# Kernel optimization log

Hardware: AMD Instinct MI355X
Metric: run time of the kernel (lower is better)

Reference implementation:

```python
import jax, jax.numpy as jnp
import numpy as np

BN_EPS = 1e-5

def conv3d(x, w, b):
    # standard 3D conv, stride 1, pad 1, NCDHW
    out = jax.lax.conv_general_dilated(x, w, (1, 1, 1), ((1, 1), (1, 1), (1, 1)),
                                       dimension_numbers=('NCDHW', 'OIDHW', 'NCDHW'))
    return out + b[None, :, None, None, None]

def batchnorm(x, gamma, beta):
    # training-mode BN over (B, D, H, W) per channel
    mu = x.mean(axis=(0, 2, 3, 4), keepdims=True)
    var = x.var(axis=(0, 2, 3, 4), keepdims=True)
    g = gamma[None, :, None, None, None]
    b = beta[None, :, None, None, None]
    return g * (x - mu) * jax.lax.rsqrt(var + BN_EPS) + b

def deform_conv3d(x, offset, weight, cpg):
    # x: [B,C,D,H,W]; offset: [B, G*27*3, D,H,W] with layout [B,G,27,(d,h,w),D,H,W]
    # weight: [C_out, C_in, 3,3,3]; kernel 3, stride 1, pad 1 -> same spatial size
    B, C, D, H, W = x.shape
    G = C // cpg
    off = offset.reshape(B, G, 27, 3, D, H, W)
    k = jnp.arange(27)
    kd = (k // 9 - 1).astype(x.dtype).reshape(1, 1, 27, 1, 1, 1)
    kh = ((k // 3) % 3 - 1).astype(x.dtype).reshape(1, 1, 27, 1, 1, 1)
    kw = (k % 3 - 1).astype(x.dtype).reshape(1, 1, 27, 1, 1, 1)
    gd = jnp.arange(D, dtype=x.dtype).reshape(1, 1, 1, D, 1, 1)
    gh = jnp.arange(H, dtype=x.dtype).reshape(1, 1, 1, 1, H, 1)
    gw = jnp.arange(W, dtype=x.dtype).reshape(1, 1, 1, 1, 1, W)
    # fractional sampling positions per (batch, group, tap, voxel): [B,G,27,D,H,W]
    pd = gd + kd + off[:, :, :, 0]
    ph = gh + kh + off[:, :, :, 1]
    pw = gw + kw + off[:, :, :, 2]
    d0 = jnp.floor(pd); h0 = jnp.floor(ph); w0 = jnp.floor(pw)
    fd = pd - d0; fh = ph - h0; fw = pw - w0
    d0i = d0.astype(jnp.int32); h0i = h0.astype(jnp.int32); w0i = w0.astype(jnp.int32)
    xg = x.reshape(B, G, cpg, D * H * W)
    N = 27 * D * H * W
    acc = jnp.zeros((B, G, cpg, 27, D, H, W), x.dtype)
    for dd in (0, 1):
        for hh in (0, 1):
            for ww in (0, 1):
                di = d0i + dd; hi = h0i + hh; wi = w0i + ww
                wgt = ((fd if dd else 1.0 - fd) * (fh if hh else 1.0 - fh)
                       * (fw if ww else 1.0 - fw))
                valid = ((di >= 0) & (di < D) & (hi >= 0) & (hi < H)
                         & (wi >= 0) & (wi < W))  # zero padding outside
                dic = jnp.clip(di, 0, D - 1)
                hic = jnp.clip(hi, 0, H - 1)
                wic = jnp.clip(wi, 0, W - 1)
                idx = ((dic * H + hic) * W + wic).reshape(B, G, 1, N)
                vals = jnp.take_along_axis(xg, jnp.broadcast_to(idx, (B, G, cpg, N)), axis=3)
                vals = vals.reshape(B, G, cpg, 27, D, H, W)
                acc = acc + (wgt * valid)[:, :, None] * vals
    wr = weight.reshape(weight.shape[0], G, cpg, 27)
    return jnp.einsum('bgckdhw,ogck->bodhw', acc, wr)

def setup_inputs() -> dict:
    key = jax.random.key(0)
    ks = jax.random.split(key, 8)
    B, C, D, H, W = 2, 64, 8, 32, 32
    cpg = 8
    Coff = (C // cpg) * 3 * 27  # 648
    fan = 1.0 / np.sqrt(C * 27)
    x = jax.random.normal(ks[0], (B, C, D, H, W), jnp.float32)
    w_off1 = jax.random.normal(ks[1], (Coff, C, 3, 3, 3), jnp.float32) * 0.01
    b_off1 = jnp.zeros((Coff,), jnp.float32)
    w1 = jax.random.normal(ks[2], (C, C, 3, 3, 3), jnp.float32) * fan
    g1 = jnp.ones((C,), jnp.float32)
    be1 = jnp.zeros((C,), jnp.float32)
    w_off2 = jax.random.normal(ks[3], (Coff, C, 3, 3, 3), jnp.float32) * 0.01
    b_off2 = jnp.zeros((Coff,), jnp.float32)
    w2 = jax.random.normal(ks[4], (C, C, 3, 3, 3), jnp.float32) * fan
    g2 = jnp.ones((C,), jnp.float32)
    be2 = jnp.zeros((C,), jnp.float32)
    return {'x': x, 'w_off1': w_off1, 'b_off1': b_off1, 'w1': w1, 'g1': g1,
            'be1': be1, 'w_off2': w_off2, 'b_off2': b_off2, 'w2': w2,
            'g2': g2, 'be2': be2, 'cpg': cpg}

def reference(x, w_off1, b_off1, w1, g1, be1, w_off2, b_off2, w2, g2, be2, cpg):
    off1 = conv3d(x, w_off1, b_off1)
    out = deform_conv3d(x, off1, w1, cpg)
    out = jax.nn.relu(batchnorm(out, g1, be1))
    off2 = conv3d(x, w_off2, b_off2)  # note: offsets computed from x, as in source
    out = deform_conv3d(out, off2, w2, cpg)
    out = batchnorm(out, g2, be2) + x
    out = jax.nn.relu(out)
    return (out, off1, off2)
```

## Files before the change

kernel.cpp:

```cpp
#include <hip/hip_runtime.h>
#include <stdint.h>

typedef unsigned short u16;
typedef __attribute__((ext_vector_type(8))) short bf16x8;
typedef __attribute__((ext_vector_type(4))) float f32x4;

#define DEV static __device__ __forceinline__

#define BB    2
#define CC    64
#define DDD   8
#define HHH   32
#define WWW   32
#define DHW   8192
#define MTOT  16384
#define GG    8
#define KTOT  1728
#define NOFF  1296
#define NOFFP 1408
#define COFF  648

#define OFF1_ELEM (BB*CC*DHW)
#define OFF2_ELEM (OFF1_ELEM + BB*COFF*DHW)

#define XCL_OFF   0ull
#define YCL_OFF   2097152ull
#define WOFF_OFF  4194304ull
#define W1_OFF    9060352ull
#define W2_OFF    9281536ull
#define C1_OFF    9502720ull
#define C2_OFF    13697024ull
#define ST1_OFF   17891328ull
#define ST2_OFF   17891840ull
#define ZPG_OFF   17892352ull
#define PART_OFF  17892608ull

DEV float bf2f(u16 u){ union { uint32_t i; float f; } v; v.i = ((uint32_t)u) << 16; return v.f; }
DEV u16 f2bf(float f){ union { float f; uint32_t i; } v; v.f = f;
  uint32_t r = v.i + 0x7fffu + ((v.i >> 16) & 1u); return (u16)(r >> 16); }

DEV void gld16(const void* g, void* l){
  __builtin_amdgcn_global_load_lds((const __attribute__((address_space(1))) void*)g,
                                   (__attribute__((address_space(3))) void*)l, 16, 0, 0);
}

__global__ void k_zero(uint32_t* z){ z[threadIdx.x] = 0u; }

__global__ void k_prep_xcl(const float* __restrict__ x, u16* __restrict__ xcl){
  int idx = blockIdx.x * 256 + threadIdx.x;
  if (idx >= BB*CC*DHW) return;
  int p = idx & (DHW - 1);
  int c = (idx >> 13) & 63;
  int b = idx >> 19;
  xcl[(size_t)(b * DHW + p) * CC + c] = f2bf(x[idx]);
}

__global__ void k_prep_woff(const float* __restrict__ wa, const float* __restrict__ wb,
                            u16* __restrict__ wo){
  int idx = blockIdx.x * 256 + threadIdx.x;
  if (idx >= NOFFP * KTOT) return;
  int k = idx % KTOT, n = idx / KTOT;
  int tap = k >> 6, cin = k & 63;
  float v = 0.f;
  if (n < NOFF) {
    const float* w = (n < COFF) ? wa : wb;
    int nn = (n < COFF) ? n : n - COFF;
    v = w[(size_t)nn * KTOT + cin * 27 + tap];
  }
  wo[idx] = f2bf(v);
}

__global__ void k_prep_w(const float* __restrict__ w, u16* __restrict__ wb){
  int idx = blockIdx.x * 256 + threadIdx.x;
  if (idx >= CC * KTOT) return;
  int k = idx % KTOT, n = idx / KTOT;
  int tap = k >> 6, cin = k & 63;
  wb[idx] = f2bf(w[(size_t)n * KTOT + cin * 27 + tap]);
}

__global__ __launch_bounds__(256) void k_gemm_off(
    const u16* __restrict__ xcl, const u16* __restrict__ woff,
    const float* __restrict__ boff1, const float* __restrict__ boff2,
    float* __restrict__ dout, const u16* __restrict__ zpg)
{
  __shared__ u16 Al[128 * 64];
  __shared__ u16 Bl[128 * 64];
  const int tid = threadIdx.x;
  const int wv = tid >> 6, lane = tid & 63;
  const int m0 = blockIdx.x * 128;
  const int n0 = blockIdx.y * 128;
  const int lr = lane >> 3, lc = lane & 7;
  const int lcs = (lc ^ lr) << 3;
  const int b  = m0 >> 13;
  const int p0 = m0 & (DHW - 1);
  int ad[4], ah[4], aw[4];
  #pragma unroll
  for (int i = 0; i < 4; ++i) {
    int p = p0 + wv * 32 + i * 8 + lr;
    ad[i] = p >> 10; ah[i] = (p >> 5) & 31; aw[i] = p & 31;
  }
  const size_t xb = (size_t)b * DHW * CC;

  f32x4 acc[4][4] = {};
  const int wm = wv >> 1, wn = wv & 1;
  const int r16 = lane & 15, q = lane >> 4;
  const int rs = r16 & 7;

  for (int t = 0; t < 27; ++t) {
    int kd = t / 9 - 1, kh = (t / 3) % 3 - 1, kw = t % 3 - 1;
    #pragma unroll
    for (int i = 0; i < 4; ++i) {
      int d2 = ad[i] + kd, h2 = ah[i] + kh, w2 = aw[i] + kw;
      bool ok = ((unsigned)d2 < DDD) & ((unsigned)h2 < HHH) & ((unsigned)w2 < WWW);
      const u16* src = ok ? (xcl + xb + (size_t)((d2 << 10) + (h2 << 5) + w2) * CC + lcs)
                          : zpg;
      gld16(src, &Al[(wv * 32 + i * 8) * 64]);
    }
    #pragma unroll
    for (int i = 0; i < 4; ++i) {
      int r = wv * 32 + i * 8 + lr;
      const u16* src = woff + (size_t)(n0 + r) * KTOT + t * 64 + lcs;
      gld16(src, &Bl[(wv * 32 + i * 8) * 64]);
    }
    __syncthreads();
    #pragma unroll
    for (int kk = 0; kk < 2; ++kk) {
      const int cs = ((kk * 4 + q) ^ rs) << 3;
      bf16x8 af[4], bfr[4];
      #pragma unroll
      for (int i = 0; i < 4; ++i)
        af[i] = *(const bf16x8*)&Al[(wm * 64 + i * 16 + r16) * 64 + cs];
      #pragma unroll
      for (int j = 0; j < 4; ++j)
        bfr[j] = *(const bf16x8*)&Bl[(wn * 64 + j * 16 + r16) * 64 + cs];
      #pragma unroll
      for (int i = 0; i < 4; ++i)
        #pragma unroll
        for (int j = 0; j < 4; ++j)
          acc[i][j] = __builtin_amdgcn_mfma_f32_16x16x32_bf16(af[i], bfr[j], acc[i][j], 0, 0, 0);
    }
    __syncthreads();
  }

  float biasj[4]; int ncj[4];
  #pragma unroll
  for (int j = 0; j < 4; ++j) {
    int nc = n0 + wn * 64 + j * 16 + r16;
    ncj[j] = nc;
    biasj[j] = (nc < NOFF) ? ((nc < COFF) ? boff1[nc] : boff2[nc - COFF]) : 0.f;
  }
  #pragma unroll
  for (int i = 0; i < 4; ++i) {
    int mrow = m0 + wm * 64 + i * 16 + q * 4;
    int bb = mrow >> 13, p = mrow & (DHW - 1);
    #pragma unroll
    for (int j = 0; j < 4; ++j) {
      int nc = ncj[j];
      if (nc < NOFF) {
        int ch = (nc < COFF) ? nc : nc - COFF;
        size_t base = (nc < COFF) ? (size_t)OFF1_ELEM : (size_t)OFF2_ELEM;
        f32x4 v = acc[i][j] + biasj[j];
        *(f32x4*)(dout + base + ((size_t)(bb * COFF + ch)) * DHW + p) = v;
      }
    }
  }
}

__global__ __launch_bounds__(256) void k_deform(
    const u16* __restrict__ src, const float* __restrict__ offs,
    const u16* __restrict__ wB, float* __restrict__ cdst)
{
  __shared__ u16 Al[32 * 64];
  __shared__ u16 Bl[64 * 64];
  const int tid = threadIdx.x;
  const int wv = tid >> 6, lane = tid & 63;
  const int mrow0 = blockIdx.x * 32;
  const int b  = mrow0 >> 13;
  const int p0 = mrow0 & (DHW - 1);

  const int pl = tid & 31;
  const int g  = tid >> 5;
  const int p  = p0 + pl;
  const int d = p >> 10, h = (p >> 5) & 31, w = p & 31;
  const u16* sb = src + (size_t)b * DHW * CC + g * 8;
  const size_t obase = ((size_t)(b * COFF + g * 81)) * DHW + p;
  const int awz = ((g ^ (pl & 7)) << 3);

  const int br_sub = lane >> 3;
  const int bcs = ((lane & 7) ^ br_sub) << 3;

  f32x4 acc[2] = {};
  const int wm = wv >> 1, wn = wv & 1;
  const int r16 = lane & 15, q = lane >> 4;
  const int rs = r16 & 7;

  for (int t = 0; t < 27; ++t) {
    int kd = t / 9 - 1, kh = (t / 3) % 3 - 1, kw = t % 3 - 1;
    #pragma unroll
    for (int k = 0; k < 2; ++k) {
      int seg = k * 4 + wv;
      int r = seg * 8 + br_sub;
      gld16(wB + (size_t)r * KTOT + t * 64 + bcs, &Bl[seg * 512]);
    }
    {
      size_t ob = obase + (size_t)(t * 3) * DHW;
      float pd = (float)(d + kd) + offs[ob];
      float ph = (float)(h + kh) + offs[ob + DHW];
      float pw = (float)(w + kw) + offs[ob + 2 * DHW];
      float fd0 = floorf(pd), fh0 = floorf(ph), fw0 = floorf(pw);
      float fd = pd - fd0, fh = ph - fh0, fw = pw - fw0;
      int d0 = (int)fd0, h0 = (int)fh0, w0 = (int)fw0;
      float a8[8] = {0.f,0.f,0.f,0.f,0.f,0.f,0.f,0.f};
      #pragma unroll
      for (int dd = 0; dd < 2; ++dd) {
        float wd = dd ? fd : 1.f - fd;
        int di = d0 + dd;
        #pragma unroll
        for (int hh = 0; hh < 2; ++hh) {
          float wh = hh ? fh : 1.f - fh;
          int hi = h0 + hh;
          #pragma unroll
          for (int ww = 0; ww < 2; ++ww) {
            int wi = w0 + ww;
            if (((unsigned)di < DDD) && ((unsigned)hi < HHH) && ((unsigned)wi < WWW)) {
              float wgt = wd * wh * (ww ? fw : 1.f - fw);
              bf16x8 v = *(const bf16x8*)(sb + (size_t)((di << 10) + (hi << 5) + wi) * CC);
              #pragma unroll
              for (int c = 0; c < 8; ++c) a8[c] += wgt * bf2f((u16)v[c]);
            }
          }
        }
      }
      union { bf16x8 v; u16 u[8]; } o;
      #pragma unroll
      for (int c = 0; c < 8; ++c) o.u[c] = f2bf(a8[c]);
      *(bf16x8*)&Al[pl * 64 + awz] = o.v;
    }
    __syncthreads();
    #pragma unroll
    for (int kk = 0; kk < 2; ++kk) {
      const int cs = ((kk * 4 + q) ^ rs) << 3;
      bf16x8 af = *(const bf16x8*)&Al[(wm * 16 + r16) * 64 + cs];
      #pragma unroll
      for (int j = 0; j < 2; ++j) {
        bf16x8 bf_ = *(const bf16x8*)&Bl[(wn * 32 + j * 16 + r16) * 64 + cs];
        acc[j] = __builtin_amdgcn_mfma_f32_16x16x32_bf16(af, bf_, acc[j], 0, 0, 0);
      }
    }
    __syncthreads();
  }

  #pragma unroll
  for (int j = 0; j < 2; ++j) {
    int nc = wn * 32 + j * 16 + r16;
    int mr = mrow0 + wm * 16 + q * 4;
    #pragma unroll
    for (int r = 0; r < 4; ++r)
      cdst[(size_t)(mr + r) * CC + nc] = acc[j][r];
  }
}

__global__ void k_bnpart(const float* __restrict__ c, float* __restrict__ part)
{
  int k = blockIdx.x, tid = threadIdx.x;
  int ch = tid & 63, sub = tid >> 6;
  float s = 0.f, s2 = 0.f;
  for (int mm = sub; mm < 64; mm += 4) {
    float v = c[(size_t)(k * 64 + mm) * CC + ch];
    s += v; s2 += v * v;
  }
  __shared__ float sh[4][128];
  sh[sub][ch] = s; sh[sub][64 + ch] = s2;
  __syncthreads();
  if (tid < 128)
    part[(size_t)k * 128 + tid] = sh[0][tid] + sh[1][tid] + sh[2][tid] + sh[3][tid];
}

__global__ void k_bnfin(const float* __restrict__ part, const float* __restrict__ gamma,
                        const float* __restrict__ beta, float* __restrict__ stats)
{
  int n = threadIdx.x;
  float S = 0.f, S2 = 0.f;
  for (int k = 0; k < 256; ++k) {
    S  += part[(size_t)k * 128 + n];
    S2 += part[(size_t)k * 128 + 64 + n];
  }
  float mu = S / (float)MTOT;
  float var = S2 / (float)MTOT - mu * mu;
  float sc = gamma[n] / sqrtf(var + 1e-5f);
  stats[n] = sc;
  stats[64 + n] = beta[n] - mu * sc;
}

__global__ void k_apply1(const float* __restrict__ c1, const float* __restrict__ st,
                         u16* __restrict__ ycl)
{
  int idx = blockIdx.x * 256 + threadIdx.x;
  if (idx >= MTOT * CC) return;
  int n = idx & 63;
  float v = st[n] * c1[idx] + st[64 + n];
  ycl[idx] = f2bf(fmaxf(v, 0.f));
}

__global__ void k_apply2(const float* __restrict__ c2, const float* __restrict__ st,
                         const float* __restrict__ x, float* __restrict__ out)
{
  int idx = blockIdx.x * 256 + threadIdx.x;
  if (idx >= BB * CC * DHW) return;
  int p = idx & (DHW - 1);
  int n = (idx >> 13) & 63;
  int b = idx >> 19;
  float v = st[n] * c2[(size_t)(b * DHW + p) * CC + n] + st[64 + n] + x[idx];
  out[idx] = fmaxf(v, 0.f);
}

extern "C" void kernel_launch(void* const* d_in, const int* in_sizes, int n_in,
                              void* d_out, int out_size, void* d_ws, size_t ws_size,
                              hipStream_t stream)
{
  (void)in_sizes; (void)n_in; (void)out_size; (void)ws_size;
  const float* x      = (const float*)d_in[0];
  const float* w_off1 = (const float*)d_in[1];
  const float* b_off1 = (const float*)d_in[2];
  const float* w1     = (const float*)d_in[3];
  const float* g1     = (const float*)d_in[4];
  const float* be1    = (const float*)d_in[5];
  const float* w_off2 = (const float*)d_in[6];
  const float* b_off2 = (const float*)d_in[7];
  const float* w2     = (const float*)d_in[8];
  const float* g2     = (const float*)d_in[9];
  const float* be2    = (const float*)d_in[10];

  char* ws = (char*)d_ws;
  u16*   xcl  = (u16*)(ws + XCL_OFF);
  u16*   ycl  = (u16*)(ws + YCL_OFF);
  u16*   woff = (u16*)(ws + WOFF_OFF);
  u16*   w1b  = (u16*)(ws + W1_OFF);
  u16*   w2b  = (u16*)(ws + W2_OFF);
  float* c1   = (float*)(ws + C1_OFF);
  float* c2   = (float*)(ws + C2_OFF);
  float* st1  = (float*)(ws + ST1_OFF);
  float* st2  = (float*)(ws + ST2_OFF);
  u16*   zpg  = (u16*)(ws + ZPG_OFF);
  float* part = (float*)(ws + PART_OFF);
  float* out  = (float*)d_out;

  k_zero<<<1, 64, 0, stream>>>((uint32_t*)zpg);
  k_prep_xcl<<<(BB*CC*DHW) / 256, 256, 0, stream>>>(x, xcl);
  k_prep_woff<<<(NOFFP * KTOT + 255) / 256, 256, 0, stream>>>(w_off1, w_off2, woff);
  k_prep_w<<<(CC * KTOT + 255) / 256, 256, 0, stream>>>(w1, w1b);
  k_prep_w<<<(CC * KTOT + 255) / 256, 256, 0, stream>>>(w2, w2b);

  k_gemm_off<<<dim3(MTOT / 128, NOFFP / 128), 256, 0, stream>>>(
      xcl, woff, b_off1, b_off2, out, zpg);

  k_deform<<<MTOT / 32, 256, 0, stream>>>(xcl, out + OFF1_ELEM, w1b, c1);
  k_bnpart<<<256, 256, 0, stream>>>(c1, part);
  k_bnfin<<<1, 64, 0, stream>>>(part, g1, be1, st1);
  k_apply1<<<(MTOT * CC) / 256, 256, 0, stream>>>(c1, st1, ycl);

  k_deform<<<MTOT / 32, 256, 0, stream>>>(ycl, out + OFF2_ELEM, w2b, c2);
  k_bnpart<<<256, 256, 0, stream>>>(c2, part);
  k_bnfin<<<1, 64, 0, stream>>>(part, g2, be2, st2);
  k_apply2<<<(BB*CC*DHW) / 256, 256, 0, stream>>>(c2, st2, x, out);
}
```

Baseline: 296.8 us.

## Double block size: deform samples two taps per step, offset GEMM uses 256-row tiles

The deformable-conv kernel now runs 512 threads. The two halves of the block each bilinearly sample a different tap into double-buffered LDS tiles, so the 27-tap loop becomes 14 phases with half as many barriers. Each of the 8 waves computes one 16x16 output tile instead of two, and the padded 28th tap is fed zeros through the zero page. The offset-conv GEMM grows to 256-row M tiles with 8 waves, splitting the B-tile loads across more waves. Together these aim to hide gather latency and cut barrier overhead, at the cost of larger LDS use per block and possibly lower occupancy.

```diff
diff --git a/kernel.cpp b/kernel.cpp
--- a/kernel.cpp
+++ b/kernel.cpp
@@ -78,16 +78,16 @@
   wb[idx] = f2bf(w[(size_t)n * KTOT + cin * 27 + tap]);
 }
 
-__global__ __launch_bounds__(256) void k_gemm_off(
+__global__ __launch_bounds__(512) void k_gemm_off(
     const u16* __restrict__ xcl, const u16* __restrict__ woff,
     const float* __restrict__ boff1, const float* __restrict__ boff2,
     float* __restrict__ dout, const u16* __restrict__ zpg)
 {
-  __shared__ u16 Al[128 * 64];
+  __shared__ u16 Al[256 * 64];
   __shared__ u16 Bl[128 * 64];
   const int tid = threadIdx.x;
   const int wv = tid >> 6, lane = tid & 63;
-  const int m0 = blockIdx.x * 128;
+  const int m0 = blockIdx.x * 256;
   const int n0 = blockIdx.y * 128;
   const int lr = lane >> 3, lc = lane & 7;
   const int lcs = (lc ^ lr) << 3;
@@ -117,10 +117,10 @@
       gld16(src, &Al[(wv * 32 + i * 8) * 64]);
     }
     #pragma unroll
-    for (int i = 0; i < 4; ++i) {
-      int r = wv * 32 + i * 8 + lr;
+    for (int i = 0; i < 2; ++i) {
+      int r = wv * 16 + i * 8 + lr;
       const u16* src = woff + (size_t)(n0 + r) * KTOT + t * 64 + lcs;
-      gld16(src, &Bl[(wv * 32 + i * 8) * 64]);
+      gld16(src, &Bl[(wv * 16 + i * 8) * 64]);
     }
     __syncthreads();
     #pragma unroll
@@ -166,12 +166,13 @@
   }
 }
 
-__global__ __launch_bounds__(256) void k_deform(
+__global__ __launch_bounds__(512) void k_deform(
     const u16* __restrict__ src, const float* __restrict__ offs,
-    const u16* __restrict__ wB, float* __restrict__ cdst)
-{
-  __shared__ u16 Al[32 * 64];
-  __shared__ u16 Bl[64 * 64];
+    const u16* __restrict__ wB, float* __restrict__ cdst,
+    const u16* __restrict__ zpg)
+{
+  __shared__ u16 Al[2 * 32 * 64];
+  __shared__ u16 Bl[2 * 64 * 64];
   const int tid = threadIdx.x;
   const int wv = tid >> 6, lane = tid & 63;
   const int mrow0 = blockIdx.x * 32;
@@ -179,54 +180,59 @@
   const int p0 = mrow0 & (DHW - 1);
 
   const int pl = tid & 31;
-  const int g  = tid >> 5;
+  const int g  = (tid >> 5) & 7;
+  const int th = tid >> 8;
   const int p  = p0 + pl;
   const int d = p >> 10, h = (p >> 5) & 31, w = p & 31;
   const u16* sb = src + (size_t)b * DHW * CC + g * 8;
   const size_t obase = ((size_t)(b * COFF + g * 81)) * DHW + p;
-  const int awz = ((g ^ (pl & 7)) << 3);
-
-  const int br_sub = lane >> 3;
-  const int bcs = ((lane & 7) ^ br_sub) << 3;
-
-  f32x4 acc[2] = {};
-  const int wm = wv >> 1, wn = wv & 1;
+  u16* awp = &Al[th * 2048 + pl * 64 + ((g ^ (pl & 7)) << 3)];
+
+  const int brow = (tid >> 3) & 63;
+  const int bch  = tid & 7;
+  const int bcs  = ((bch ^ (brow & 7)) << 3);
+
+  f32x4 acc = {};
+  const int wm = wv >> 2, wn = wv & 3;
   const int r16 = lane & 15, q = lane >> 4;
   const int rs = r16 & 7;
 
-  for (int t = 0; t < 27; ++t) {
-    int kd = t / 9 - 1, kh = (t / 3) % 3 - 1, kw = t % 3 - 1;
-    #pragma unroll
-    for (int k = 0; k < 2; ++k) {
-      int seg = k * 4 + wv;
-      int r = seg * 8 + br_sub;
-      gld16(wB + (size_t)r * KTOT + t * 64 + bcs, &Bl[seg * 512]);
+  for (int ph = 0; ph < 14; ++ph) {
+    #pragma unroll
+    for (int i = 0; i < 2; ++i) {
+      int tb = 2 * ph + i;
+      const u16* s = (tb < 27) ? (wB + (size_t)brow * KTOT + tb * 64 + bcs) : zpg;
+      gld16(s, &Bl[(i * 512 + wv * 64) * 8]);
     }
     {
-      size_t ob = obase + (size_t)(t * 3) * DHW;
-      float pd = (float)(d + kd) + offs[ob];
-      float ph = (float)(h + kh) + offs[ob + DHW];
-      float pw = (float)(w + kw) + offs[ob + 2 * DHW];
-      float fd0 = floorf(pd), fh0 = floorf(ph), fw0 = floorf(pw);
-      float fd = pd - fd0, fh = ph - fh0, fw = pw - fw0;
-      int d0 = (int)fd0, h0 = (int)fh0, w0 = (int)fw0;
+      int t = 2 * ph + th;
       float a8[8] = {0.f,0.f,0.f,0.f,0.f,0.f,0.f,0.f};
-      #pragma unroll
-      for (int dd = 0; dd < 2; ++dd) {
-        float wd = dd ? fd : 1.f - fd;
-        int di = d0 + dd;
+      if (t < 27) {
+        int kd = t / 9 - 1, kh = (t / 3) % 3 - 1, kw = t % 3 - 1;
+        size_t ob = obase + (size_t)(t * 3) * DHW;
+        float pd = (float)(d + kd) + offs[ob];
+        float phh = (float)(h + kh) + offs[ob + DHW];
+        float pw = (float)(w + kw) + offs[ob + 2 * DHW];
+        float fd0 = floorf(pd), fh0 = floorf(phh), fw0 = floorf(pw);
+        float fd = pd - fd0, fh = phh - fh0, fw = pw - fw0;
+        int d0 = (int)fd0, h0 = (int)fh0, w0 = (int)fw0;
         #pragma unroll
-        for (int hh = 0; hh < 2; ++hh) {
-          float wh = hh ? fh : 1.f - fh;
-          int hi = h0 + hh;
+        for (int dd = 0; dd < 2; ++dd) {
+          float wd = dd ? fd : 1.f - fd;
+          int di = d0 + dd;
           #pragma unroll
-          for (int ww = 0; ww < 2; ++ww) {
-            int wi = w0 + ww;
-            if (((unsigned)di < DDD) && ((unsigned)hi < HHH) && ((unsigned)wi < WWW)) {
-              float wgt = wd * wh * (ww ? fw : 1.f - fw);
-              bf16x8 v = *(const bf16x8*)(sb + (size_t)((di << 10) + (hi << 5) + wi) * CC);
-              #pragma unroll
-              for (int c = 0; c < 8; ++c) a8[c] += wgt * bf2f((u16)v[c]);
+          for (int hh = 0; hh < 2; ++hh) {
+            float wh = hh ? fh : 1.f - fh;
+            int hi = h0 + hh;
+            #pragma unroll
+            for (int ww = 0; ww < 2; ++ww) {
+              int wi = w0 + ww;
+              if (((unsigned)di < DDD) && ((unsigned)hi < HHH) && ((unsigned)wi < WWW)) {
+                float wgt = wd * wh * (ww ? fw : 1.f - fw);
+                bf16x8 v = *(const bf16x8*)(sb + (size_t)((di << 10) + (hi << 5) + wi) * CC);
+                #pragma unroll
+                for (int c = 0; c < 8; ++c) a8[c] += wgt * bf2f((u16)v[c]);
+              }
             }
           }
         }
@@ -234,29 +240,28 @@
       union { bf16x8 v; u16 u[8]; } o;
       #pragma unroll
       for (int c = 0; c < 8; ++c) o.u[c] = f2bf(a8[c]);
-      *(bf16x8*)&Al[pl * 64 + awz] = o.v;
+      *(bf16x8*)awp = o.v;
     }
     __syncthreads();
     #pragma unroll
-    for (int kk = 0; kk < 2; ++kk) {
-      const int cs = ((kk * 4 + q) ^ rs) << 3;
-      bf16x8 af = *(const bf16x8*)&Al[(wm * 16 + r16) * 64 + cs];
-      #pragma unroll
-      for (int j = 0; j < 2; ++j) {
-        bf16x8 bf_ = *(const bf16x8*)&Bl[(wn * 32 + j * 16 + r16) * 64 + cs];
-        acc[j] = __builtin_amdgcn_mfma_f32_16x16x32_bf16(af, bf_, acc[j], 0, 0, 0);
+    for (int tt = 0; tt < 2; ++tt) {
+      #pragma unroll
+      for (int kk = 0; kk < 2; ++kk) {
+        const int cs = ((kk * 4 + q) ^ rs) << 3;
+        bf16x8 af = *(const bf16x8*)&Al[tt * 2048 + (wm * 16 + r16) * 64 + cs];
+        bf16x8 bf_ = *(const bf16x8*)&Bl[tt * 4096 + (wn * 16 + r16) * 64 + cs];
+        acc = __builtin_amdgcn_mfma_f32_16x16x32_bf16(af, bf_, acc, 0, 0, 0);
       }
     }
     __syncthreads();
   }
 
-  #pragma unroll
-  for (int j = 0; j < 2; ++j) {
-    int nc = wn * 32 + j * 16 + r16;
+  {
+    int nc = wn * 16 + r16;
     int mr = mrow0 + wm * 16 + q * 4;
     #pragma unroll
     for (int r = 0; r < 4; ++r)
-      cdst[(size_t)(mr + r) * CC + nc] = acc[j][r];
+      cdst[(size_t)(mr + r) * CC + nc] = acc[r];
   }
 }
 
@@ -351,15 +356,15 @@
   k_prep_w<<<(CC * KTOT + 255) / 256, 256, 0, stream>>>(w1, w1b);
   k_prep_w<<<(CC * KTOT + 255) / 256, 256, 0, stream>>>(w2, w2b);
 
-  k_gemm_off<<<dim3(MTOT / 128, NOFFP / 128), 256, 0, stream>>>(
+  k_gemm_off<<<dim3(MTOT / 256, NOFFP / 128), 512, 0, stream>>>(
       xcl, woff, b_off1, b_off2, out, zpg);
 
-  k_deform<<<MTOT / 32, 256, 0, stream>>>(xcl, out + OFF1_ELEM, w1b, c1);
+  k_deform<<<MTOT / 32, 512, 0, stream>>>(xcl, out + OFF1_ELEM, w1b, c1, zpg);
   k_bnpart<<<256, 256, 0, stream>>>(c1, part);
   k_bnfin<<<1, 64, 0, stream>>>(part, g1, be1, st1);
   k_apply1<<<(MTOT * CC) / 256, 256, 0, stream>>>(c1, st1, ycl);
 
-  k_deform<<<MTOT / 32, 256, 0, stream>>>(ycl, out + OFF2_ELEM, w2b, c2);
+  k_deform<<<MTOT / 32, 512, 0, stream>>>(ycl, out + OFF2_ELEM, w2b, c2, zpg);
   k_bnpart<<<256, 256, 0, stream>>>(c2, part);
   k_bnfin<<<1, 64, 0, stream>>>(part, g2, be2, st2);
   k_apply2<<<(BB*CC*DHW) / 256, 256, 0, stream>>>(c2, st2, x, out);
```

Measured after the change: 278.4 us. -6.2%, faster.
